# Kernel tuning notes

Measured on AMD Instinct MI355X. Metric: run time of the kernel, lower is better.

The kernel has to match this reference:

```python
import jax, jax.numpy as jnp
import numpy as np

HEADS = 16
DIM_HEAD = 64
SCALE = DIM_HEAD ** -0.5


def setup_inputs() -> dict:
    key = jax.random.key(0)
    ks = jax.random.split(key, 7)
    b, n, m, d = 2, 2048, 2048, 1024
    inner = HEADS * DIM_HEAD  # 1024
    patch_embed = jax.random.normal(ks[0], (b, n, d), dtype=jnp.float32)
    pixel_embed = jax.random.normal(ks[1], (b, m, d), dtype=jnp.float32)
    s = 1.0 / np.sqrt(d)
    Wq = jax.random.normal(ks[2], (d, inner), dtype=jnp.float32) * s
    Wk = jax.random.normal(ks[3], (d, inner), dtype=jnp.float32) * s
    Wv = jax.random.normal(ks[4], (d, inner), dtype=jnp.float32) * s
    Wo = jax.random.normal(ks[5], (inner, d), dtype=jnp.float32) * (1.0 / np.sqrt(inner))
    bo = jax.random.normal(ks[6], (d,), dtype=jnp.float32) * 0.01
    return {"patch_embed": patch_embed, "pixel_embed": pixel_embed,
            "Wq": Wq, "Wk": Wk, "Wv": Wv, "Wo": Wo, "bo": bo}


def reference(patch_embed, pixel_embed, Wq, Wk, Wv, Wo, bo):
    b, n, _ = patch_embed.shape
    h, dh = HEADS, DIM_HEAD
    # projections
    q = patch_embed @ Wq  # [b, n, h*dh]
    k = pixel_embed @ Wk  # [b, m, h*dh]
    v = pixel_embed @ Wv  # [b, m, h*dh]
    # split heads: [b, seq, h, dh]
    q = q.reshape(b, n, h, dh)
    k = k.reshape(b, -1, h, dh)
    v = v.reshape(b, -1, h, dh)
    sim = jnp.einsum('bihd,bjhd->bhij', q, k) * SCALE  # [b, h, n, m]
    attn = jax.nn.softmax(sim, axis=-1)
    out = jnp.einsum('bhij,bjhd->bihd', attn, v)  # [b, n, h, dh]
    out = out.reshape(b, n, h * dh)
    return out @ Wo + bo  # [b, n, query_dim]
```

## Files before the change

### kernel.cpp

```cpp
#include <hip/hip_runtime.h>

#define SEQ 2048
#define DMODEL 1024
#define HEADS 16
#define DH 64
#define QSCALE 0.180336880f

typedef __attribute__((ext_vector_type(8))) short short8;
typedef __attribute__((ext_vector_type(4))) float f32x4;

__device__ __forceinline__ ushort f2bf(float x) {
  union { float f; unsigned u; } v; v.f = x;
  return (ushort)((v.u + 0x7fffu + ((v.u >> 16) & 1u)) >> 16);
}

__device__ __forceinline__ void gld16(const ushort* g, ushort* l) {
  __builtin_amdgcn_global_load_lds(
      (const __attribute__((address_space(1))) unsigned int*)g,
      (__attribute__((address_space(3))) unsigned int*)l, 16, 0, 0);
}

__device__ __forceinline__ size_t qk_idx(int bh, int s, int d) {
  return ((((size_t)bh * (SEQ / 16) + (s >> 4)) * 2 + (d >> 5)) * 64 +
          ((d >> 3) & 3) * 16 + (s & 15)) * 8 + (d & 7);
}
__device__ __forceinline__ size_t v_idx(int bh, int s, int d) {
  return ((((size_t)bh * (SEQ / 32) + (s >> 5)) * 4 + (d >> 4)) * 64 +
          ((s >> 3) & 3) * 16 + (d & 15)) * 8 + (s & 7);
}

__global__ __launch_bounds__(256) void prologue(
    const float* __restrict__ patch, const float* __restrict__ pixel,
    const float* __restrict__ W0, const float* __restrict__ W1,
    const float* __restrict__ W2, const float* __restrict__ W3,
    ushort* __restrict__ pb, ushort* __restrict__ xb,
    ushort* __restrict__ O0, ushort* __restrict__ O1,
    ushort* __restrict__ O2, ushort* __restrict__ O3) {
  const int z = blockIdx.z;
  const int tx = threadIdx.x, ty = threadIdx.y;
  if (z < 2) {
    const float4* in = (const float4*)(z ? pixel : patch);
    ushort4* out = (ushort4*)(z ? xb : pb);
    const int base = (blockIdx.y * 32 + blockIdx.x) * 256 + ty * 32 + tx;
#pragma unroll
    for (int rep = 0; rep < 4; ++rep) {
      const int i = base + rep * 262144;
      float4 f = in[i];
      out[i] = make_ushort4(f2bf(f.x), f2bf(f.y), f2bf(f.z), f2bf(f.w));
    }
    return;
  }
  __shared__ float tile[32][33];
  const int zz = z - 2;
  const float* in = zz == 0 ? W0 : zz == 1 ? W1 : zz == 2 ? W2 : W3;
  ushort* out = zz == 0 ? O0 : zz == 1 ? O1 : zz == 2 ? O2 : O3;
  const float scale = zz == 0 ? QSCALE : 1.0f;
  const int n0 = blockIdx.x * 32, k0 = blockIdx.y * 32;
#pragma unroll
  for (int i = 0; i < 4; ++i)
    tile[ty + i * 8][tx] = in[(size_t)(k0 + ty + i * 8) * DMODEL + n0 + tx];
  __syncthreads();
#pragma unroll
  for (int i = 0; i < 4; ++i)
    out[(size_t)(n0 + ty + i * 8) * DMODEL + k0 + tx] =
        f2bf(tile[tx][ty + i * 8] * scale);
}

__global__ __launch_bounds__(256) void mfma_gemm_qkv(
    const ushort* __restrict__ pb, const ushort* __restrict__ xb,
    const ushort* __restrict__ wqt, const ushort* __restrict__ wkt,
    const ushort* __restrict__ wvt, ushort* __restrict__ qws,
    ushort* __restrict__ kws, ushort* __restrict__ vws) {
  __shared__ __align__(16) ushort As[128 * 64];
  __shared__ __align__(16) ushort Bs[128 * 64];
  const int z = blockIdx.z;
  const ushort* A = (z == 0) ? pb : xb;
  const ushort* Bt = (z == 0) ? wqt : (z == 1) ? wkt : wvt;

  const int t = threadIdx.x;
  const int w = t >> 6, lane = t & 63, ln = lane & 15, q = lane >> 4;
  const int wm = w & 1, wn = w >> 1;
  const int row0 = blockIdx.y * 128, col0 = blockIdx.x * 128;
  const int sw = ln & 7;

  f32x4 acc[4][4];
#pragma unroll
  for (int i = 0; i < 4; ++i)
#pragma unroll
    for (int j = 0; j < 4; ++j) acc[i][j] = (f32x4){0.f, 0.f, 0.f, 0.f};

  for (int k0 = 0; k0 < DMODEL; k0 += 64) {
    __syncthreads();
#pragma unroll
    for (int rep = 0; rep < 4; ++rep) {
      const int u0 = rep * 256 + w * 64;
      const int u = u0 + lane;
      const int r = u >> 3, gl = (u & 7) ^ (r & 7);
      gld16(&A[(size_t)(row0 + r) * DMODEL + k0 + gl * 8], &As[u0 * 8]);
      gld16(&Bt[(size_t)(col0 + r) * DMODEL + k0 + gl * 8], &Bs[u0 * 8]);
    }
    __syncthreads();
#pragma unroll
    for (int ks = 0; ks < 2; ++ks) {
      short8 af[4], bf[4];
#pragma unroll
      for (int rt = 0; rt < 4; ++rt)
        af[rt] = *(const short8*)&As[(wm * 64 + rt * 16 + ln) * 64 +
                                     (((ks * 4 + q) ^ sw) * 8)];
#pragma unroll
      for (int ct = 0; ct < 4; ++ct)
        bf[ct] = *(const short8*)&Bs[(wn * 64 + ct * 16 + ln) * 64 +
                                     (((ks * 4 + q) ^ sw) * 8)];
#pragma unroll
      for (int rt = 0; rt < 4; ++rt)
#pragma unroll
        for (int ct = 0; ct < 4; ++ct)
          acc[rt][ct] = __builtin_amdgcn_mfma_f32_16x16x32_bf16(af[rt], bf[ct],
                                                                acc[rt][ct], 0, 0, 0);
    }
  }

  if (z < 2) {
    ushort* dst = z == 0 ? qws : kws;
#pragma unroll
    for (int rt = 0; rt < 4; ++rt)
#pragma unroll
      for (int ct = 0; ct < 4; ++ct) {
        const int c = col0 + wn * 64 + ct * 16 + ln;
        const int h = c >> 6, d = c & 63;
#pragma unroll
        for (int reg = 0; reg < 4; ++reg) {
          const int r = row0 + wm * 64 + rt * 16 + q * 4 + reg;
          const int b = r >> 11, s = r & (SEQ - 1);
          dst[qk_idx(b * HEADS + h, s, d)] = f2bf(acc[rt][ct][reg]);
        }
      }
  } else {
#pragma unroll
    for (int rt = 0; rt < 4; ++rt)
#pragma unroll
      for (int ct = 0; ct < 4; ++ct) {
        const int c = col0 + wn * 64 + ct * 16 + ln;
        const int h = c >> 6, d = c & 63;
        const int r0 = row0 + wm * 64 + rt * 16 + q * 4;
        const int b = r0 >> 11, s0 = r0 & (SEQ - 1);
        ushort4 u4 = make_ushort4(f2bf(acc[rt][ct][0]), f2bf(acc[rt][ct][1]),
                                  f2bf(acc[rt][ct][2]), f2bf(acc[rt][ct][3]));
        *(ushort4*)&vws[v_idx(b * HEADS + h, s0, d)] = u4;
      }
  }
}

__global__ __launch_bounds__(256, 4) void flash_mfma(
    const ushort* __restrict__ Qg, const ushort* __restrict__ Kg,
    const ushort* __restrict__ Vg, ushort* __restrict__ Og) {
  __shared__ __align__(16) ushort Kst[2][8 * 512];
  __shared__ __align__(16) ushort Ps[64 * 76];

  const int t = threadIdx.x;
  const int w = t >> 6, lane = t & 63, ln = lane & 15, q = lane >> 4;
  const int bh = blockIdx.x;
  const int qt = blockIdx.y;

  const ushort* qg = Qg + (size_t)bh * SEQ * DH;
  const ushort* kg = Kg + (size_t)bh * SEQ * DH;
  const ushort* vg = Vg + (size_t)bh * DH * SEQ;

  short8 qf[2];
#pragma unroll
  for (int ks = 0; ks < 2; ++ks)
    qf[ks] = *(const short8*)
        &qg[(((size_t)(qt * 4 + w) * 2 + ks) * 64 + lane) * 8];

  float l_i[4] = {0.f, 0.f, 0.f, 0.f};
  f32x4 acc_o[4];
#pragma unroll
  for (int nt = 0; nt < 4; ++nt) acc_o[nt] = (f32x4){0.f, 0.f, 0.f, 0.f};

#pragma unroll
  for (int i = 0; i < 2; ++i) {
    const int f = w * 2 + i;
    gld16(&kg[(size_t)f * 512 + lane * 8], &Kst[0][f * 512]);
  }
  __syncthreads();

  for (int kt = 0; kt < SEQ / 64; ++kt) {
    const int cur = kt & 1;
    if (kt + 1 < SEQ / 64) {
#pragma unroll
      for (int i = 0; i < 2; ++i) {
        const int f = w * 2 + i;
        gld16(&kg[(size_t)((kt + 1) * 8 + f) * 512 + lane * 8],
              &Kst[cur ^ 1][f * 512]);
      }
    }

    short8 bv[2][4];
#pragma unroll
    for (int ks2 = 0; ks2 < 2; ++ks2)
#pragma unroll
      for (int nt = 0; nt < 4; ++nt)
        bv[ks2][nt] = *(const short8*)
            &vg[((size_t)((kt * 2 + ks2) * 4 + nt) * 64 + lane) * 8];

    f32x4 accs[4];
#pragma unroll
    for (int ct = 0; ct < 4; ++ct) accs[ct] = (f32x4){0.f, 0.f, 0.f, 0.f};
#pragma unroll
    for (int ks = 0; ks < 2; ++ks)
#pragma unroll
      for (int ct = 0; ct < 4; ++ct) {
        const short8 bfr = *(const short8*)&Kst[cur][(ct * 2 + ks) * 512 + lane * 8];
        accs[ct] = __builtin_amdgcn_mfma_f32_16x16x32_bf16(
            qf[ks], bfr, accs[ct], 0, 0, 0);
      }

#pragma unroll
    for (int ct = 0; ct < 4; ++ct)
#pragma unroll
      for (int reg = 0; reg < 4; ++reg) {
        const float p = __builtin_amdgcn_exp2f(accs[ct][reg]);
        l_i[reg] += p;
        union { float f; unsigned u; } v; v.f = p;
        Ps[(w * 16 + q * 4 + reg) * 76 + ct * 16 + ln] =
            (ushort)((v.u + 0x8000u) >> 16);
      }

#pragma unroll
    for (int ks2 = 0; ks2 < 2; ++ks2) {
      const short8 pa = *(const short8*)&Ps[(w * 16 + ln) * 76 + ks2 * 32 + q * 8];
#pragma unroll
      for (int nt = 0; nt < 4; ++nt)
        acc_o[nt] = __builtin_amdgcn_mfma_f32_16x16x32_bf16(
            pa, bv[ks2][nt], acc_o[nt], 0, 0, 0);
    }

    __syncthreads();
  }

  const int b = bh >> 4, h = bh & 15;
#pragma unroll
  for (int reg = 0; reg < 4; ++reg) {
    float l = l_i[reg];
    l += __shfl_xor(l, 1, 16);
    l += __shfl_xor(l, 2, 16);
    l += __shfl_xor(l, 4, 16);
    l += __shfl_xor(l, 8, 16);
    const float inv = 1.0f / l;
    const int s = qt * 64 + w * 16 + q * 4 + reg;
#pragma unroll
    for (int nt = 0; nt < 4; ++nt)
      Og[(size_t)(b * SEQ + s) * DMODEL + h * DH + nt * 16 + ln] =
          f2bf(acc_o[nt][reg] * inv);
  }
}

__global__ __launch_bounds__(256) void mfma_gemm_out(const ushort* __restrict__ A,
                                                     const ushort* __restrict__ Bt,
                                                     const float* __restrict__ bias,
                                                     float* __restrict__ dst) {
  __shared__ __align__(16) ushort As[64 * 64];
  __shared__ __align__(16) ushort Bs[128 * 64];
  const int t = threadIdx.x;
  const int w = t >> 6, lane = t & 63, ln = lane & 15, q = lane >> 4;
  const int wm = w & 1, wn = w >> 1;
  const int row0 = blockIdx.y * 64, col0 = blockIdx.x * 128;
  const int sw = ln & 7;

  f32x4 acc[2][4];
#pragma unroll
  for (int i = 0; i < 2; ++i)
#pragma unroll
    for (int j = 0; j < 4; ++j) acc[i][j] = (f32x4){0.f, 0.f, 0.f, 0.f};

  for (int k0 = 0; k0 < DMODEL; k0 += 64) {
    __syncthreads();
#pragma unroll
    for (int rep = 0; rep < 2; ++rep) {
      const int u0 = rep * 256 + w * 64;
      const int u = u0 + lane;
      const int r = u >> 3, gl = (u & 7) ^ (r & 7);
      gld16(&A[(size_t)(row0 + r) * DMODEL + k0 + gl * 8], &As[u0 * 8]);
    }
#pragma unroll
    for (int rep = 0; rep < 4; ++rep) {
      const int u0 = rep * 256 + w * 64;
      const int u = u0 + lane;
      const int r = u >> 3, gl = (u & 7) ^ (r & 7);
      gld16(&Bt[(size_t)(col0 + r) * DMODEL + k0 + gl * 8], &Bs[u0 * 8]);
    }
    __syncthreads();
#pragma unroll
    for (int ks = 0; ks < 2; ++ks) {
      short8 af[2], bf[4];
#pragma unroll
      for (int rt = 0; rt < 2; ++rt)
        af[rt] = *(const short8*)&As[(wm * 32 + rt * 16 + ln) * 64 +
                                     (((ks * 4 + q) ^ sw) * 8)];
#pragma unroll
      for (int ct = 0; ct < 4; ++ct)
        bf[ct] = *(const short8*)&Bs[(wn * 64 + ct * 16 + ln) * 64 +
                                     (((ks * 4 + q) ^ sw) * 8)];
#pragma unroll
      for (int rt = 0; rt < 2; ++rt)
#pragma unroll
        for (int ct = 0; ct < 4; ++ct)
          acc[rt][ct] = __builtin_amdgcn_mfma_f32_16x16x32_bf16(af[rt], bf[ct],
                                                                acc[rt][ct], 0, 0, 0);
    }
  }

#pragma unroll
  for (int rt = 0; rt < 2; ++rt)
#pragma unroll
    for (int ct = 0; ct < 4; ++ct) {
      const int c = col0 + wn * 64 + ct * 16 + ln;
      const float bi = bias[c];
#pragma unroll
      for (int reg = 0; reg < 4; ++reg) {
        const int r = row0 + wm * 32 + rt * 16 + q * 4 + reg;
        dst[(size_t)r * DMODEL + c] = acc[rt][ct][reg] + bi;
      }
    }
}

extern "C" void kernel_launch(void* const* d_in, const int* in_sizes, int n_in,
                              void* d_out, int out_size, void* d_ws,
                              size_t ws_size, hipStream_t stream) {
  const float* patch = (const float*)d_in[0];
  const float* pixel = (const float*)d_in[1];
  const float* Wq = (const float*)d_in[2];
  const float* Wk = (const float*)d_in[3];
  const float* Wv = (const float*)d_in[4];
  const float* Wo = (const float*)d_in[5];
  const float* bo = (const float*)d_in[6];
  float* out = (float*)d_out;

  const size_t E = (size_t)2 * SEQ * DMODEL;
  const size_t W = (size_t)DMODEL * DMODEL;
  ushort* pb  = (ushort*)d_ws;
  ushort* xb  = pb + E;
  ushort* wqt = xb + E;
  ushort* wkt = wqt + W;
  ushort* wvt = wkt + W;
  ushort* wot = wvt + W;
  ushort* qws = wot + W;
  ushort* kws = qws + E;
  ushort* vws = kws + E;
  ushort* aws = vws + E;

  prologue<<<dim3(32, 32, 6), dim3(32, 8), 0, stream>>>(
      patch, pixel, Wq, Wk, Wv, Wo, pb, xb, wqt, wkt, wvt, wot);
  mfma_gemm_qkv<<<dim3(8, 32, 3), 256, 0, stream>>>(pb, xb, wqt, wkt, wvt,
                                                    qws, kws, vws);
  flash_mfma<<<dim3(32, 32), 256, 0, stream>>>(qws, kws, vws, aws);
  mfma_gemm_out<<<dim3(8, 64), 256, 0, stream>>>(aws, wot, bo, out);
}
```

Measured before the change: 208.1 us.

## Rework flash attention around 32x32x16 MFMA with in-register P and LDS-staged V

The attention kernel moves from 16x16x32 to 32x32x16 bf16 MFMA tiles with 128 query rows per block. Softmax probabilities are packed with v_cvt_pk_bf16_f32 and rearranged via permlane32_swap, so the P round trip through LDS is gone. V is now staged in swizzled LDS via async global-to-LDS loads, split between warps, instead of being read directly from global. Q/K are stored in plain row-major layout and V transposed, and occupancy is reduced to 2 blocks per CU, trading occupancy for larger tiles and more reuse.

```diff
diff --git a/kernel.cpp b/kernel.cpp
--- a/kernel.cpp
+++ b/kernel.cpp
@@ -8,6 +8,9 @@
 
 typedef __attribute__((ext_vector_type(8))) short short8;
 typedef __attribute__((ext_vector_type(4))) float f32x4;
+typedef __attribute__((ext_vector_type(16))) float f32x16;
+typedef __attribute__((ext_vector_type(2))) unsigned int uint2v;
+typedef __attribute__((ext_vector_type(4))) unsigned int uint4v;
 
 __device__ __forceinline__ ushort f2bf(float x) {
   union { float f; unsigned u; } v; v.f = x;
@@ -18,15 +21,6 @@
   __builtin_amdgcn_global_load_lds(
       (const __attribute__((address_space(1))) unsigned int*)g,
       (__attribute__((address_space(3))) unsigned int*)l, 16, 0, 0);
-}
-
-__device__ __forceinline__ size_t qk_idx(int bh, int s, int d) {
-  return ((((size_t)bh * (SEQ / 16) + (s >> 4)) * 2 + (d >> 5)) * 64 +
-          ((d >> 3) & 3) * 16 + (s & 15)) * 8 + (d & 7);
-}
-__device__ __forceinline__ size_t v_idx(int bh, int s, int d) {
-  return ((((size_t)bh * (SEQ / 32) + (s >> 5)) * 4 + (d >> 4)) * 64 +
-          ((s >> 3) & 3) * 16 + (d & 15)) * 8 + (s & 7);
 }
 
 __global__ __launch_bounds__(256) void prologue(
@@ -127,12 +121,10 @@
 #pragma unroll
       for (int ct = 0; ct < 4; ++ct) {
         const int c = col0 + wn * 64 + ct * 16 + ln;
-        const int h = c >> 6, d = c & 63;
 #pragma unroll
         for (int reg = 0; reg < 4; ++reg) {
           const int r = row0 + wm * 64 + rt * 16 + q * 4 + reg;
-          const int b = r >> 11, s = r & (SEQ - 1);
-          dst[qk_idx(b * HEADS + h, s, d)] = f2bf(acc[rt][ct][reg]);
+          dst[(size_t)r * DMODEL + c] = f2bf(acc[rt][ct][reg]);
         }
       }
   } else {
@@ -141,46 +133,59 @@
 #pragma unroll
       for (int ct = 0; ct < 4; ++ct) {
         const int c = col0 + wn * 64 + ct * 16 + ln;
-        const int h = c >> 6, d = c & 63;
+        const int hh = c >> 6, d = c & 63;
         const int r0 = row0 + wm * 64 + rt * 16 + q * 4;
-        const int b = r0 >> 11, s0 = r0 & (SEQ - 1);
+        const int bb = r0 >> 11, s0 = r0 & (SEQ - 1);
         ushort4 u4 = make_ushort4(f2bf(acc[rt][ct][0]), f2bf(acc[rt][ct][1]),
                                   f2bf(acc[rt][ct][2]), f2bf(acc[rt][ct][3]));
-        *(ushort4*)&vws[v_idx(b * HEADS + h, s0, d)] = u4;
-      }
-  }
-}
-
-__global__ __launch_bounds__(256, 4) void flash_mfma(
+        *(ushort4*)&vws[((size_t)(bb * HEADS + hh) * DH + d) * SEQ + s0] = u4;
+      }
+  }
+}
+
+__global__ __launch_bounds__(256, 2) void flash_mfma(
     const ushort* __restrict__ Qg, const ushort* __restrict__ Kg,
     const ushort* __restrict__ Vg, ushort* __restrict__ Og) {
-  __shared__ __align__(16) ushort Kst[2][8 * 512];
-  __shared__ __align__(16) ushort Ps[64 * 76];
+  __shared__ __align__(16) ushort Kst[2][64 * 64];
+  __shared__ __align__(16) ushort Vst[2][64 * 64];
 
   const int t = threadIdx.x;
-  const int w = t >> 6, lane = t & 63, ln = lane & 15, q = lane >> 4;
+  const int w = t >> 6, lane = t & 63;
+  const int l31 = lane & 31, hi = lane >> 5, l7 = lane & 7, l8 = lane >> 3;
   const int bh = blockIdx.x;
   const int qt = blockIdx.y;
-
-  const ushort* qg = Qg + (size_t)bh * SEQ * DH;
-  const ushort* kg = Kg + (size_t)bh * SEQ * DH;
+  const int b = bh >> 4, h = bh & 15;
+
+  const ushort* qrow = Qg + ((size_t)b * SEQ) * DMODEL + h * DH;
+  const ushort* krow = Kg + ((size_t)b * SEQ) * DMODEL + h * DH;
   const ushort* vg = Vg + (size_t)bh * DH * SEQ;
 
-  short8 qf[2];
-#pragma unroll
-  for (int ks = 0; ks < 2; ++ks)
+  short8 qf[4];
+#pragma unroll
+  for (int ks = 0; ks < 4; ++ks)
     qf[ks] = *(const short8*)
-        &qg[(((size_t)(qt * 4 + w) * 2 + ks) * 64 + lane) * 8];
-
-  float l_i[4] = {0.f, 0.f, 0.f, 0.f};
-  f32x4 acc_o[4];
-#pragma unroll
-  for (int nt = 0; nt < 4; ++nt) acc_o[nt] = (f32x4){0.f, 0.f, 0.f, 0.f};
-
-#pragma unroll
-  for (int i = 0; i < 2; ++i) {
-    const int f = w * 2 + i;
-    gld16(&kg[(size_t)f * 512 + lane * 8], &Kst[0][f * 512]);
+        &qrow[(size_t)(qt * 128 + w * 32 + l31) * DMODEL + ks * 16 + hi * 8];
+
+  f32x16 acc_o[2];
+#pragma unroll
+  for (int db = 0; db < 2; ++db)
+#pragma unroll
+    for (int e = 0; e < 16; ++e) acc_o[db][e] = 0.f;
+  float l_i = 0.f;
+
+  const int fbase = (w & 1) * 4;
+  const bool isV = (w >= 2);
+  const int swz = (l7 ^ l8) * 8;
+
+  {
+#pragma unroll
+    for (int i = 0; i < 4; ++i) {
+      const int f = fbase + i;
+      if (!isV)
+        gld16(&krow[(size_t)(f * 8 + l8) * DMODEL + swz], &Kst[0][f * 512]);
+      else
+        gld16(&vg[(size_t)(f * 8 + l8) * SEQ + swz], &Vst[0][f * 512]);
+    }
   }
   __syncthreads();
 
@@ -188,71 +193,102 @@
     const int cur = kt & 1;
     if (kt + 1 < SEQ / 64) {
 #pragma unroll
-      for (int i = 0; i < 2; ++i) {
-        const int f = w * 2 + i;
-        gld16(&kg[(size_t)((kt + 1) * 8 + f) * 512 + lane * 8],
-              &Kst[cur ^ 1][f * 512]);
-      }
-    }
-
-    short8 bv[2][4];
-#pragma unroll
-    for (int ks2 = 0; ks2 < 2; ++ks2)
-#pragma unroll
-      for (int nt = 0; nt < 4; ++nt)
-        bv[ks2][nt] = *(const short8*)
-            &vg[((size_t)((kt * 2 + ks2) * 4 + nt) * 64 + lane) * 8];
-
-    f32x4 accs[4];
-#pragma unroll
-    for (int ct = 0; ct < 4; ++ct) accs[ct] = (f32x4){0.f, 0.f, 0.f, 0.f};
-#pragma unroll
-    for (int ks = 0; ks < 2; ++ks)
-#pragma unroll
-      for (int ct = 0; ct < 4; ++ct) {
-        const short8 bfr = *(const short8*)&Kst[cur][(ct * 2 + ks) * 512 + lane * 8];
-        accs[ct] = __builtin_amdgcn_mfma_f32_16x16x32_bf16(
-            qf[ks], bfr, accs[ct], 0, 0, 0);
-      }
-
-#pragma unroll
-    for (int ct = 0; ct < 4; ++ct)
-#pragma unroll
-      for (int reg = 0; reg < 4; ++reg) {
-        const float p = __builtin_amdgcn_exp2f(accs[ct][reg]);
-        l_i[reg] += p;
-        union { float f; unsigned u; } v; v.f = p;
-        Ps[(w * 16 + q * 4 + reg) * 76 + ct * 16 + ln] =
-            (ushort)((v.u + 0x8000u) >> 16);
-      }
-
-#pragma unroll
-    for (int ks2 = 0; ks2 < 2; ++ks2) {
-      const short8 pa = *(const short8*)&Ps[(w * 16 + ln) * 76 + ks2 * 32 + q * 8];
-#pragma unroll
-      for (int nt = 0; nt < 4; ++nt)
-        acc_o[nt] = __builtin_amdgcn_mfma_f32_16x16x32_bf16(
-            pa, bv[ks2][nt], acc_o[nt], 0, 0, 0);
-    }
-
-    __syncthreads();
-  }
-
-  const int b = bh >> 4, h = bh & 15;
-#pragma unroll
-  for (int reg = 0; reg < 4; ++reg) {
-    float l = l_i[reg];
-    l += __shfl_xor(l, 1, 16);
-    l += __shfl_xor(l, 2, 16);
-    l += __shfl_xor(l, 4, 16);
-    l += __shfl_xor(l, 8, 16);
-    const float inv = 1.0f / l;
-    const int s = qt * 64 + w * 16 + q * 4 + reg;
-#pragma unroll
-    for (int nt = 0; nt < 4; ++nt)
-      Og[(size_t)(b * SEQ + s) * DMODEL + h * DH + nt * 16 + ln] =
-          f2bf(acc_o[nt][reg] * inv);
-  }
+      for (int i = 0; i < 4; ++i) {
+        const int f = fbase + i;
+        if (!isV)
+          gld16(&krow[(size_t)((kt + 1) * 64 + f * 8 + l8) * DMODEL + swz],
+                &Kst[cur ^ 1][f * 512]);
+        else
+          gld16(&vg[(size_t)(f * 8 + l8) * SEQ + (kt + 1) * 64 + swz],
+                &Vst[cur ^ 1][f * 512]);
+      }
+    }
+
+    const ushort* Kc = &Kst[cur][0];
+    const ushort* Vc = &Vst[cur][0];
+
+    f32x16 accs[2];
+#pragma unroll
+    for (int kb = 0; kb < 2; ++kb)
+#pragma unroll
+      for (int e = 0; e < 16; ++e) accs[kb][e] = 0.f;
+#pragma unroll
+    for (int kb = 0; kb < 2; ++kb)
+#pragma unroll
+      for (int ks = 0; ks < 4; ++ks) {
+        const short8 kf = *(const short8*)
+            &Kc[(kb * 32 + l31) * 64 + (((ks * 2 + hi) ^ l7) * 8)];
+        accs[kb] = __builtin_amdgcn_mfma_f32_32x32x16_bf16(kf, qf[ks],
+                                                           accs[kb], 0, 0, 0);
+      }
+
+    short8 vf[4][2];
+#pragma unroll
+    for (int sg = 0; sg < 4; ++sg)
+#pragma unroll
+      for (int db = 0; db < 2; ++db)
+        vf[sg][db] = *(const short8*)
+            &Vc[(db * 32 + l31) * 64 + (((sg * 2 + hi) ^ l7) * 8)];
+
+#pragma unroll
+    for (int kb = 0; kb < 2; ++kb)
+#pragma unroll
+      for (int e = 0; e < 16; ++e) {
+        const float p = __builtin_amdgcn_exp2f(accs[kb][e]);
+        accs[kb][e] = p;
+        l_i += p;
+      }
+
+    short8 pa[4];
+#pragma unroll
+    for (int kb = 0; kb < 2; ++kb) {
+      unsigned wq[4][2];
+#pragma unroll
+      for (int o = 0; o < 4; ++o) {
+        asm("v_cvt_pk_bf16_f32 %0, %1, %2"
+            : "=v"(wq[o][0])
+            : "v"(accs[kb][4 * o + 0]), "v"(accs[kb][4 * o + 1]));
+        asm("v_cvt_pk_bf16_f32 %0, %1, %2"
+            : "=v"(wq[o][1])
+            : "v"(accs[kb][4 * o + 2]), "v"(accs[kb][4 * o + 3]));
+      }
+#pragma unroll
+      for (int sl = 0; sl < 2; ++sl) {
+        uint2v r02 = __builtin_amdgcn_permlane32_swap(wq[2 * sl][0],
+                                                      wq[2 * sl + 1][0],
+                                                      false, false);
+        uint2v r13 = __builtin_amdgcn_permlane32_swap(wq[2 * sl][1],
+                                                      wq[2 * sl + 1][1],
+                                                      false, false);
+        uint4v pk = {r02.x, r13.x, r02.y, r13.y};
+        pa[kb * 2 + sl] = __builtin_bit_cast(short8, pk);
+      }
+    }
+
+#pragma unroll
+    for (int sg = 0; sg < 4; ++sg)
+#pragma unroll
+      for (int db = 0; db < 2; ++db)
+        acc_o[db] = __builtin_amdgcn_mfma_f32_32x32x16_bf16(pa[sg], vf[sg][db],
+                                                            acc_o[db], 0, 0, 0);
+
+    __syncthreads();
+  }
+
+  l_i += __shfl_xor(l_i, 32);
+  const float inv = 1.0f / l_i;
+#pragma unroll
+  for (int o = 0; o < 4; ++o)
+#pragma unroll
+    for (int r0 = 0; r0 < 4; ++r0) {
+      const int row = o * 8 + r0 + 4 * hi;
+      const float invr = __shfl(inv, row, 64);
+      const int s = qt * 128 + w * 32 + row;
+#pragma unroll
+      for (int db = 0; db < 2; ++db)
+        Og[(size_t)(b * SEQ + s) * DMODEL + h * DH + db * 32 + l31] =
+            f2bf(acc_o[db][4 * o + r0] * invr);
+    }
 }
 
 __global__ __launch_bounds__(256) void mfma_gemm_out(const ushort* __restrict__ A,
@@ -353,6 +389,6 @@
       patch, pixel, Wq, Wk, Wv, Wo, pb, xb, wqt, wkt, wvt, wot);
   mfma_gemm_qkv<<<dim3(8, 32, 3), 256, 0, stream>>>(pb, xb, wqt, wkt, wvt,
                                                     qws, kws, vws);
-  flash_mfma<<<dim3(32, 32), 256, 0, stream>>>(qws, kws, vws, aws);
+  flash_mfma<<<dim3(32, 16), 256, 0, stream>>>(qws, kws, vws, aws);
   mfma_gemm_out<<<dim3(8, 64), 256, 0, stream>>>(aws, wot, bo, out);
 }
```

Measured after the change: 190.8 us. 1.09x faster.
